# Kernel optimization log

Hardware: AMD Instinct MI355X
Metric: run time of the kernel (lower is better)

## Reference

```python
import jax, jax.numpy as jnp
import numpy as np

E = 8          # num_experts
K = 2          # top_k
D = 1024       # hidden_size
I = 4096       # intermediate_size
AUX_COEF = 0.02


def setup_inputs() -> dict:
    key = jax.random.key(0)
    ks = jax.random.split(key, 5)
    x = jax.random.normal(ks[0], (4, 2048, D), dtype=jnp.float32)
    w_gate = jax.random.normal(ks[1], (E, D), dtype=jnp.float32) * 0.02   # router, nn.Linear weight [E, D]
    wg = jax.random.normal(ks[2], (E, D, I), dtype=jnp.float32) * 0.02    # gate_proj per expert
    wu = jax.random.normal(ks[3], (E, D, I), dtype=jnp.float32) * 0.02    # up_proj per expert
    wd = jax.random.normal(ks[4], (E, I, D), dtype=jnp.float32) * 0.02    # down_proj per expert
    return {"x": x, "w_gate": w_gate, "wg": wg, "wu": wu, "wd": wd}


def reference(x, w_gate, wg, wu, wd):
    B, T, Dm = x.shape
    xf = x.reshape(-1, Dm)                                   # [N, D]
    N = xf.shape[0]

    # 1) Router: softmax (in fp32) + top-k, renormalize top-k weights
    logits = xf @ w_gate.T                                   # [N, E]
    probs = jax.nn.softmax(logits.astype(jnp.float32), axis=-1)
    topk_w, topk_idx = jax.lax.top_k(probs, K)               # [N, K]
    topk_w = (topk_w / topk_w.sum(-1, keepdims=True)).astype(x.dtype)

    # Per-expert combine weight (zero when expert not selected) — math-equivalent
    # to the original gather/scatter-add loop but jit-friendly and vectorized.
    onehot = jax.nn.one_hot(topk_idx, E, dtype=x.dtype)      # [N, K, E]
    combine = jnp.einsum('nk,nke->ne', topk_w, onehot)       # [N, E]

    # 2) Experts: SwiGLU FFN, combined with routing weights
    out = jnp.zeros_like(xf)
    for e in range(E):  # fixed small loop over structurally distinct experts
        h = jax.nn.silu(xf @ wg[e]) * (xf @ wu[e])           # [N, I]
        out = out + combine[:, e:e + 1] * (h @ wd[e])        # [N, D]

    # 3) Load-balancing aux loss (Switch Transformer)
    f = onehot.sum((0, 1)).astype(jnp.float32) / (N * K)     # dispatch fraction per expert
    p = probs.mean(0)                                        # mean routing prob per expert
    aux_loss = AUX_COEF * E * jnp.sum(f * p)

    return out.reshape(B, T, Dm), aux_loss
```

## Files before the change

### kernel.cpp

```cpp
#include <hip/hip_runtime.h>
#include <hip/hip_bf16.h>
#include <cstdint>
#include <cstddef>

#define NE 8
#define TK 2
#define DM 1024
#define IM 4096
#define NT 8192
#define NS (NT*TK)
#define SCAP (NS+256)

typedef __bf16 bf16_t;
typedef __bf16 bf16x8 __attribute__((ext_vector_type(8)));
typedef __bf16 bf16x4 __attribute__((ext_vector_type(4)));
typedef float f32x4 __attribute__((ext_vector_type(4)));

__device__ __forceinline__ void async_cp16(const bf16_t* g, bf16_t* l) {
  __builtin_amdgcn_global_load_lds(
      (__attribute__((address_space(1))) void*)(const_cast<bf16_t*>(g)),
      (__attribute__((address_space(3))) void*)(l), 16, 0, 0);
}

__global__ void transpose_cvt(const float* __restrict__ src, bf16_t* __restrict__ dst,
                              int R, int C) {
  __shared__ float t[32][33];
  int bx = blockIdx.x * 32, by = blockIdx.y * 32;
  size_t zb = (size_t)blockIdx.z * R * C;
  int tx = threadIdx.x, ty = threadIdx.y;
#pragma unroll
  for (int i = 0; i < 4; ++i)
    t[ty + i*8][tx] = src[zb + (size_t)(by + ty + i*8) * C + bx + tx];
  __syncthreads();
#pragma unroll
  for (int i = 0; i < 4; ++i)
    dst[zb + (size_t)(bx + ty + i*8) * R + by + tx] = (bf16_t)t[tx][ty + i*8];
}

__global__ void pack_gu(const float* __restrict__ wg, const float* __restrict__ wu,
                        bf16_t* __restrict__ Wgu) {
  __shared__ float t[32][33];
  int sel = blockIdx.z & 1, e = blockIdx.z >> 1;
  const float* src = sel ? wu : wg;
  size_t zb = (size_t)e * DM * IM;
  int bx = blockIdx.x * 32, by = blockIdx.y * 32;
  int tx = threadIdx.x, ty = threadIdx.y;
#pragma unroll
  for (int i = 0; i < 4; ++i)
    t[ty + i*8][tx] = src[zb + (size_t)(by + ty + i*8) * IM + bx + tx];
  __syncthreads();
#pragma unroll
  for (int i = 0; i < 4; ++i) {
    int icol = bx + ty + i*8;
    int p = ((icol >> 6) << 7) + (sel << 6) + (icol & 63);
    Wgu[((size_t)e * (2*IM) + p) * DM + by + tx] = (bf16_t)t[tx][ty + i*8];
  }
}

__global__ void router_kernel(const float* __restrict__ x, const float* __restrict__ wgate,
                              int* __restrict__ counts, float* __restrict__ prob_sum,
                              int* __restrict__ topk_idx, float* __restrict__ topk_w) {
  __shared__ float s_psum[NE];
  __shared__ int s_cnt[NE];
  int tid = threadIdx.x;
  if (tid < NE) { s_psum[tid] = 0.f; s_cnt[tid] = 0; }
  __syncthreads();
  int lane = tid & 63, wv = tid >> 6;
  for (int t = 0; t < 8; ++t) {
    int n = blockIdx.x * 32 + wv * 8 + t;
    float acc[NE];
#pragma unroll
    for (int e = 0; e < NE; ++e) acc[e] = 0.f;
#pragma unroll
    for (int j = 0; j < 16; ++j) {
      int d = j * 64 + lane;
      float xv = x[(size_t)n * DM + d];
#pragma unroll
      for (int e = 0; e < NE; ++e) acc[e] += xv * wgate[e * DM + d];
    }
#pragma unroll
    for (int e = 0; e < NE; ++e) {
#pragma unroll
      for (int off = 32; off > 0; off >>= 1) acc[e] += __shfl_xor(acc[e], off);
    }
    if (lane == 0) {
      float mx = acc[0];
#pragma unroll
      for (int e = 1; e < NE; ++e) mx = fmaxf(mx, acc[e]);
      float p[NE], s = 0.f;
#pragma unroll
      for (int e = 0; e < NE; ++e) { p[e] = __expf(acc[e] - mx); s += p[e]; }
      float inv = 1.f / s;
#pragma unroll
      for (int e = 0; e < NE; ++e) p[e] *= inv;
      int i0 = 0;
      for (int e = 1; e < NE; ++e) if (p[e] > p[i0]) i0 = e;
      int i1 = (i0 == 0) ? 1 : 0;
      for (int e = 0; e < NE; ++e) if (e != i0 && p[e] > p[i1]) i1 = e;
      float rs = 1.f / (p[i0] + p[i1]);
      topk_idx[n * 2 + 0] = i0; topk_idx[n * 2 + 1] = i1;
      topk_w[n * 2 + 0] = p[i0] * rs; topk_w[n * 2 + 1] = p[i1] * rs;
      atomicAdd(&s_cnt[i0], 1); atomicAdd(&s_cnt[i1], 1);
#pragma unroll
      for (int e = 0; e < NE; ++e) atomicAdd(&s_psum[e], p[e]);
    }
  }
  __syncthreads();
  if (tid < NE) { atomicAdd(&counts[tid], s_cnt[tid]); atomicAdd(&prob_sum[tid], s_psum[tid]); }
}

__global__ void scan_aux(const int* __restrict__ counts, const float* __restrict__ prob_sum,
                         int* __restrict__ offsets, int* __restrict__ cursors,
                         float* __restrict__ aux_out) {
  if (threadIdx.x == 0) {
    int off = 0;
    float aux = 0.f;
    for (int e = 0; e < NE; ++e) {
      offsets[e] = off; cursors[e] = off;
      float f = (float)counts[e] * (1.f / (float)NS);
      float p = prob_sum[e] * (1.f / (float)NT);
      aux += f * p;
      off += counts[e];
    }
    offsets[NE] = off;
    *aux_out = 0.02f * 8.f * aux;
  }
}

__global__ void gather_kernel(const float* __restrict__ x, const int* __restrict__ topk_idx,
                              const float* __restrict__ topk_w, int* __restrict__ cursors,
                              int* __restrict__ slot_token, float* __restrict__ slot_w,
                              int* __restrict__ pair_slot, bf16_t* __restrict__ Xg) {
  int lane = threadIdx.x & 63, wv = threadIdx.x >> 6;
  int pair = blockIdx.x * 4 + wv;
  int n = pair >> 1, k = pair & 1;
  int e = topk_idx[n * 2 + k];
  int slot = 0;
  if (lane == 0) slot = atomicAdd(&cursors[e], 1);
  slot = __shfl(slot, 0);
  if (lane == 0) {
    slot_token[slot] = n; slot_w[slot] = topk_w[n * 2 + k];
    pair_slot[pair] = slot;
  }
#pragma unroll
  for (int j = 0; j < 4; ++j) {
    int d4 = j * 256 + lane * 4;
    float4 v = *(const float4*)(x + (size_t)n * DM + d4);
    bf16x4 o;
    o[0] = (bf16_t)v.x; o[1] = (bf16_t)v.y; o[2] = (bf16_t)v.z; o[3] = (bf16_t)v.w;
    *(bf16x4*)(Xg + (size_t)slot * DM + d4) = o;
  }
}

#define MFMA16 __builtin_amdgcn_mfma_f32_16x16x32_bf16

__global__ __launch_bounds__(512, 2) void gemm1_kernel(
    const bf16_t* __restrict__ Xg, const bf16_t* __restrict__ Wgu,
    bf16_t* __restrict__ H, const int* __restrict__ offsets) {
  int e = blockIdx.z, mt = blockIdx.y, nt = blockIdx.x;
  int row0 = offsets[e], ne = offsets[e + 1] - row0;
  if (mt * 256 >= ne) return;
  int m0 = row0 + mt * 256;

  __shared__ bf16_t lds[2][4][128 * 64];

  int tid = threadIdx.x, lane = tid & 63, wv = tid >> 6;
  int fm = lane & 15, fq = lane >> 4;
  int wm = wv >> 2, wn = wv & 3;

  const bf16_t* Ab = Xg + (size_t)m0 * DM;
  const bf16_t* Bb = Wgu + ((size_t)e * (2 * IM) + nt * 256) * DM;

  int sr = tid >> 3;
  int sgc = ((tid & 7) ^ (sr & 7)) << 3;
  int sldo = tid * 8;

#define STAGE1(LDST, GBASE, COL) do {                                      \
    const bf16_t* _g = (GBASE);                                            \
    async_cp16(_g + (size_t)sr * DM + (COL) + sgc, (LDST) + sldo);         \
    async_cp16(_g + (size_t)(sr + 64) * DM + (COL) + sgc, (LDST) + sldo + 4096); \
  } while (0)

  int offA[4][2], offB[2][2];
#pragma unroll
  for (int m = 0; m < 4; ++m) {
    int r = m * 32 + wm * 16 + fm;
#pragma unroll
    for (int ks = 0; ks < 2; ++ks)
      offA[m][ks] = r * 64 + (((ks * 4 + fq) ^ (r & 7)) << 3);
  }
#pragma unroll
  for (int jh = 0; jh < 2; ++jh) {
    int r = jh * 64 + wn * 16 + fm;
#pragma unroll
    for (int ks = 0; ks < 2; ++ks)
      offB[jh][ks] = r * 64 + (((ks * 4 + fq) ^ (r & 7)) << 3);
  }

  f32x4 acc[8][4];
#pragma unroll
  for (int i = 0; i < 8; ++i)
#pragma unroll
    for (int j = 0; j < 4; ++j) acc[i][j] = (f32x4){0.f, 0.f, 0.f, 0.f};

  STAGE1(lds[0][0], Ab, 0);
  STAGE1(lds[0][2], Bb, 0);
  STAGE1(lds[0][3], Bb + (size_t)128 * DM, 0);
  STAGE1(lds[0][1], Ab + (size_t)128 * DM, 0);
  STAGE1(lds[1][0], Ab, 64);
  STAGE1(lds[1][2], Bb, 64);
  STAGE1(lds[1][3], Bb + (size_t)128 * DM, 64);
  asm volatile("s_waitcnt vmcnt(6)");
  __builtin_amdgcn_s_barrier();

  bf16x8 af[4][2], b0f[2][2], b1f[2][2];
#pragma unroll 1
  for (int t = 0; t < 16; ++t) {
    const int buf = t & 1;
    const bf16_t* LA0 = lds[buf][0];
    const bf16_t* LA1 = lds[buf][1];
    const bf16_t* LB0 = lds[buf][2];
    const bf16_t* LB1 = lds[buf][3];
#pragma unroll
    for (int m = 0; m < 4; ++m) {
      af[m][0] = *(const bf16x8*)(LA0 + offA[m][0]);
      af[m][1] = *(const bf16x8*)(LA0 + offA[m][1]);
    }
#pragma unroll
    for (int j = 0; j < 2; ++j) {
      b0f[j][0] = *(const bf16x8*)(LB0 + offB[j][0]);
      b0f[j][1] = *(const bf16x8*)(LB0 + offB[j][1]);
    }
    if (t + 1 < 16) STAGE1(lds[buf ^ 1][1], Ab + (size_t)128 * DM, (t + 1) * 64);
    __builtin_amdgcn_s_barrier();
    asm volatile("s_waitcnt lgkmcnt(0)");
    __builtin_amdgcn_sched_barrier(0);
    __builtin_amdgcn_s_setprio(1);
#pragma unroll
    for (int m = 0; m < 4; ++m)
#pragma unroll
      for (int j = 0; j < 2; ++j) {
        acc[m][j] = MFMA16(af[m][0], b0f[j][0], acc[m][j], 0, 0, 0);
        acc[m][j] = MFMA16(af[m][1], b0f[j][1], acc[m][j], 0, 0, 0);
      }
    __builtin_amdgcn_s_setprio(0);
    __builtin_amdgcn_s_barrier();
#pragma unroll
    for (int j = 0; j < 2; ++j) {
      b1f[j][0] = *(const bf16x8*)(LB1 + offB[j][0]);
      b1f[j][1] = *(const bf16x8*)(LB1 + offB[j][1]);
    }
    if (t + 2 < 16) STAGE1(lds[buf][0], Ab, (t + 2) * 64);
    __builtin_amdgcn_s_barrier();
    asm volatile("s_waitcnt lgkmcnt(0)");
    __builtin_amdgcn_sched_barrier(0);
    __builtin_amdgcn_s_setprio(1);
#pragma unroll
    for (int m = 0; m < 4; ++m)
#pragma unroll
      for (int j = 0; j < 2; ++j) {
        acc[m][2 + j] = MFMA16(af[m][0], b1f[j][0], acc[m][2 + j], 0, 0, 0);
        acc[m][2 + j] = MFMA16(af[m][1], b1f[j][1], acc[m][2 + j], 0, 0, 0);
      }
    __builtin_amdgcn_s_setprio(0);
    __builtin_amdgcn_s_barrier();
#pragma unroll
    for (int m = 0; m < 4; ++m) {
      af[m][0] = *(const bf16x8*)(LA1 + offA[m][0]);
      af[m][1] = *(const bf16x8*)(LA1 + offA[m][1]);
    }
    if (t + 2 < 16) STAGE1(lds[buf][2], Bb, (t + 2) * 64);
    __builtin_amdgcn_s_barrier();
    asm volatile("s_waitcnt lgkmcnt(0)");
    __builtin_amdgcn_sched_barrier(0);
    __builtin_amdgcn_s_setprio(1);
#pragma unroll
    for (int m = 0; m < 4; ++m)
#pragma unroll
      for (int j = 0; j < 2; ++j) {
        acc[4 + m][j] = MFMA16(af[m][0], b0f[j][0], acc[4 + m][j], 0, 0, 0);
        acc[4 + m][j] = MFMA16(af[m][1], b0f[j][1], acc[4 + m][j], 0, 0, 0);
      }
    __builtin_amdgcn_s_setprio(0);
    __builtin_amdgcn_s_barrier();
    if (t + 2 < 16) STAGE1(lds[buf][3], Bb + (size_t)128 * DM, (t + 2) * 64);
    if (t < 14) { asm volatile("s_waitcnt vmcnt(6)"); }
    else if (t == 14) { asm volatile("s_waitcnt vmcnt(0)"); }
    __builtin_amdgcn_s_barrier();
    __builtin_amdgcn_s_setprio(1);
#pragma unroll
    for (int m = 0; m < 4; ++m)
#pragma unroll
      for (int j = 0; j < 2; ++j) {
        acc[4 + m][2 + j] = MFMA16(af[m][0], b1f[j][0], acc[4 + m][2 + j], 0, 0, 0);
        acc[4 + m][2 + j] = MFMA16(af[m][1], b1f[j][1], acc[4 + m][2 + j], 0, 0, 0);
      }
    __builtin_amdgcn_s_setprio(0);
    __builtin_amdgcn_s_barrier();
  }
#undef STAGE1

#pragma unroll
  for (int i = 0; i < 8; ++i) {
    int lr = i * 32 + wm * 16 + fq * 4;
#pragma unroll
    for (int rr = 0; rr < 4; ++rr) {
      if (mt * 256 + lr + rr < ne) {
        bf16_t* hp = H + (size_t)(m0 + lr + rr) * IM + nt * 128 + wn * 16 + fm;
        float g0 = acc[i][0][rr], u0 = acc[i][1][rr];
        hp[0] = (bf16_t)(g0 * __builtin_amdgcn_rcpf(1.f + __expf(-g0)) * u0);
        float g1 = acc[i][2][rr], u1 = acc[i][3][rr];
        hp[64] = (bf16_t)(g1 * __builtin_amdgcn_rcpf(1.f + __expf(-g1)) * u1);
      }
    }
  }
}

__global__ __launch_bounds__(256, 2) void gemm2_kernel(
    const bf16_t* __restrict__ H, const bf16_t* __restrict__ Wdt,
    const int* __restrict__ offsets, bf16_t* __restrict__ Y) {
  int e = blockIdx.z, mt = blockIdx.y, nt = blockIdx.x;
  int row0 = offsets[e], ne = offsets[e + 1] - row0;
  if (mt * 128 >= ne) return;
  int m0 = row0 + mt * 128;
  int n0 = nt * 128;

  __shared__ bf16_t sA[128 * 64];
  __shared__ bf16_t sB[128 * 64];

  int tid = threadIdx.x, lane = tid & 63, wv = tid >> 6;
  int fm = lane & 15, fq = lane >> 4;
  int wm = (wv & 1) * 64, wn = (wv >> 1) * 64;

  f32x4 acc[4][4];
#pragma unroll
  for (int i = 0; i < 4; ++i)
#pragma unroll
    for (int j = 0; j < 4; ++j) acc[i][j] = (f32x4){0.f, 0.f, 0.f, 0.f};

  const bf16_t* Ab = H + (size_t)m0 * IM;
  const bf16_t* Bb = Wdt + ((size_t)e * DM + n0) * IM;

  for (int k0 = 0; k0 < IM; k0 += 64) {
    __syncthreads();
#pragma unroll
    for (int it = 0; it < 4; ++it) {
      int c = it * 256 + tid;
      int r = c >> 3, c8 = c & 7;
      int gc8 = c8 ^ (r & 7);
      size_t go = (size_t)r * IM + k0 + gc8 * 8;
      async_cp16(Ab + go, sA + c * 8);
      async_cp16(Bb + go, sB + c * 8);
    }
    __syncthreads();
#pragma unroll
    for (int s = 0; s < 2; ++s) {
      bf16x8 af[4], bf[4];
      int q = s * 4 + fq;
#pragma unroll
      for (int i = 0; i < 4; ++i) {
        int ra = wm + i * 16 + fm;
        int rb = wn + i * 16 + fm;
        af[i] = *(const bf16x8*)(sA + ra * 64 + (q ^ (ra & 7)) * 8);
        bf[i] = *(const bf16x8*)(sB + rb * 64 + (q ^ (rb & 7)) * 8);
      }
#pragma unroll
      for (int i = 0; i < 4; ++i)
#pragma unroll
        for (int j = 0; j < 4; ++j)
          acc[i][j] = __builtin_amdgcn_mfma_f32_16x16x32_bf16(af[i], bf[j], acc[i][j], 0, 0, 0);
    }
  }
#pragma unroll
  for (int i = 0; i < 4; ++i) {
#pragma unroll
    for (int r = 0; r < 4; ++r) {
      int lm = wm + i * 16 + fq * 4 + r;
      if (mt * 128 + lm < ne) {
        bf16_t* yrow = Y + (size_t)(m0 + lm) * DM + n0 + wn;
#pragma unroll
        for (int j = 0; j < 4; ++j)
          yrow[j * 16 + fm] = (bf16_t)acc[i][j][r];
      }
    }
  }
}

__global__ void combine_kernel(const bf16_t* __restrict__ Y, const int* __restrict__ pair_slot,
                               const float* __restrict__ topk_w, float* __restrict__ out) {
  int n = blockIdx.x;
  int t = threadIdx.x;
  int s0 = pair_slot[n * 2 + 0], s1 = pair_slot[n * 2 + 1];
  float w0 = topk_w[n * 2 + 0], w1 = topk_w[n * 2 + 1];
  bf16x4 y0 = *(const bf16x4*)(Y + (size_t)s0 * DM + t * 4);
  bf16x4 y1 = *(const bf16x4*)(Y + (size_t)s1 * DM + t * 4);
  float4 o;
  o.x = w0 * (float)y0[0] + w1 * (float)y1[0];
  o.y = w0 * (float)y0[1] + w1 * (float)y1[1];
  o.z = w0 * (float)y0[2] + w1 * (float)y1[2];
  o.w = w0 * (float)y0[3] + w1 * (float)y1[3];
  *(float4*)(out + (size_t)n * DM + t * 4) = o;
}

static constexpr size_t OFF_TOPKI = 256;
static constexpr size_t OFF_TOPKW = OFF_TOPKI + (size_t)NT * 2 * 4;
static constexpr size_t OFF_STOK  = OFF_TOPKW + (size_t)NT * 2 * 4;
static constexpr size_t OFF_SW    = OFF_STOK + (size_t)NS * 4;
static constexpr size_t OFF_PSLOT = OFF_SW + (size_t)NS * 4;
static constexpr size_t OFF_XG    = OFF_PSLOT + (size_t)NS * 4;
static constexpr size_t OFF_H     = OFF_XG + (size_t)SCAP * DM * 2;
static constexpr size_t OFF_WGU   = OFF_H + (size_t)SCAP * IM * 2;
static constexpr size_t OFF_WDT   = OFF_WGU + (size_t)NE * 2 * IM * DM * 2;

extern "C" void kernel_launch(void* const* d_in, const int* in_sizes, int n_in,
                              void* d_out, int out_size, void* d_ws, size_t ws_size,
                              hipStream_t stream) {
  const float* x      = (const float*)d_in[0];
  const float* w_gate = (const float*)d_in[1];
  const float* wg     = (const float*)d_in[2];
  const float* wu     = (const float*)d_in[3];
  const float* wd     = (const float*)d_in[4];
  float* out = (float*)d_out;

  char* ws = (char*)d_ws;
  int*   counts   = (int*)(ws + 0);
  int*   cursors  = (int*)(ws + 32);
  int*   offsets  = (int*)(ws + 64);
  float* prob_sum = (float*)(ws + 128);
  int*   topk_idx = (int*)(ws + OFF_TOPKI);
  float* topk_w   = (float*)(ws + OFF_TOPKW);
  int*   slot_tok = (int*)(ws + OFF_STOK);
  float* slot_w   = (float*)(ws + OFF_SW);
  int*   pair_slot= (int*)(ws + OFF_PSLOT);
  bf16_t* Xg  = (bf16_t*)(ws + OFF_XG);
  bf16_t* Yb  = Xg;
  bf16_t* Hb  = (bf16_t*)(ws + OFF_H);
  bf16_t* Wgu = (bf16_t*)(ws + OFF_WGU);
  bf16_t* Wdt = (bf16_t*)(ws + OFF_WDT);

  hipMemsetAsync(ws, 0, 256, stream);

  pack_gu<<<dim3(IM / 32, DM / 32, NE * 2), dim3(32, 8), 0, stream>>>(wg, wu, Wgu);
  transpose_cvt<<<dim3(DM / 32, IM / 32, NE), dim3(32, 8), 0, stream>>>(wd, Wdt, IM, DM);

  router_kernel<<<NT / 32, 256, 0, stream>>>(x, w_gate, counts, prob_sum, topk_idx, topk_w);
  scan_aux<<<1, 64, 0, stream>>>(counts, prob_sum, offsets, cursors, out + (out_size - 1));
  gather_kernel<<<NS / 4, 256, 0, stream>>>(x, topk_idx, topk_w, cursors, slot_tok, slot_w,
                                            pair_slot, Xg);

  gemm1_kernel<<<dim3(IM / 128, 64, NE), 512, 0, stream>>>(Xg, Wgu, Hb, offsets);
  gemm2_kernel<<<dim3(DM / 128, 64, NE), 256, 0, stream>>>(Hb, Wdt, offsets, Yb);
  combine_kernel<<<NT, 256, 0, stream>>>(Yb, pair_slot, topk_w, out);
}
```

Measured before the change: 1.234 ms.

## Unify MoE GEMMs into templated pipelined kernel with compact tile list

After: 1.183 ms. -4.1%, faster.

```diff
diff --git a/kernel.cpp b/kernel.cpp
--- a/kernel.cpp
+++ b/kernel.cpp
@@ -10,6 +10,7 @@
 #define NT 8192
 #define NS (NT*TK)
 #define SCAP (NS+256)
+#define MAXT 72
 
 typedef __bf16 bf16_t;
 typedef __bf16 bf16x8 __attribute__((ext_vector_type(8)));
@@ -111,18 +112,28 @@
 
 __global__ void scan_aux(const int* __restrict__ counts, const float* __restrict__ prob_sum,
                          int* __restrict__ offsets, int* __restrict__ cursors,
-                         float* __restrict__ aux_out) {
+                         float* __restrict__ aux_out, int* __restrict__ tl_m0,
+                         int* __restrict__ tl_e, int* __restrict__ tl_rows,
+                         int* __restrict__ n_tiles) {
   if (threadIdx.x == 0) {
     int off = 0;
     float aux = 0.f;
+    int t = 0;
     for (int e = 0; e < NE; ++e) {
       offsets[e] = off; cursors[e] = off;
-      float f = (float)counts[e] * (1.f / (float)NS);
+      int c = counts[e];
+      float f = (float)c * (1.f / (float)NS);
       float p = prob_sum[e] * (1.f / (float)NT);
       aux += f * p;
-      off += counts[e];
+      for (int m = 0; m * 256 < c && t < MAXT; ++m, ++t) {
+        tl_m0[t] = off + m * 256;
+        tl_e[t] = e;
+        tl_rows[t] = min(256, c - m * 256);
+      }
+      off += c;
     }
     offsets[NE] = off;
+    *n_tiles = t;
     *aux_out = 0.02f * 8.f * aux;
   }
 }
@@ -153,14 +164,22 @@
 }
 
 #define MFMA16 __builtin_amdgcn_mfma_f32_16x16x32_bf16
-
-__global__ __launch_bounds__(512, 2) void gemm1_kernel(
-    const bf16_t* __restrict__ Xg, const bf16_t* __restrict__ Wgu,
-    bf16_t* __restrict__ H, const int* __restrict__ offsets) {
-  int e = blockIdx.z, mt = blockIdx.y, nt = blockIdx.x;
-  int row0 = offsets[e], ne = offsets[e + 1] - row0;
-  if (mt * 256 >= ne) return;
-  int m0 = row0 + mt * 256;
+#define SBAR  __builtin_amdgcn_s_barrier
+#define SCHED __builtin_amdgcn_sched_barrier
+#define PRIO  __builtin_amdgcn_s_setprio
+
+template<int NTK, int KSTR, int BROWS, bool SWIGLU>
+__global__ __launch_bounds__(512, 2) void moe_gemm(
+    const bf16_t* __restrict__ A, const bf16_t* __restrict__ Bw,
+    bf16_t* __restrict__ O,
+    const int* __restrict__ tl_m0, const int* __restrict__ tl_e,
+    const int* __restrict__ tl_rows, const int* __restrict__ n_tiles) {
+  int ty = blockIdx.y;
+  if (ty >= *n_tiles) return;
+  int m0 = tl_m0[ty];
+  int e  = tl_e[ty];
+  int rows = tl_rows[ty];
+  int nt = blockIdx.x;
 
   __shared__ bf16_t lds[2][4][128 * 64];
 
@@ -168,17 +187,17 @@
   int fm = lane & 15, fq = lane >> 4;
   int wm = wv >> 2, wn = wv & 3;
 
-  const bf16_t* Ab = Xg + (size_t)m0 * DM;
-  const bf16_t* Bb = Wgu + ((size_t)e * (2 * IM) + nt * 256) * DM;
+  const bf16_t* Ab = A + (size_t)m0 * KSTR;
+  const bf16_t* Bb = Bw + ((size_t)e * BROWS + (size_t)nt * 256) * KSTR;
 
   int sr = tid >> 3;
   int sgc = ((tid & 7) ^ (sr & 7)) << 3;
   int sldo = tid * 8;
 
-#define STAGE1(LDST, GBASE, COL) do {                                      \
+#define STG(LDST, GBASE, COL) do {                                         \
     const bf16_t* _g = (GBASE);                                            \
-    async_cp16(_g + (size_t)sr * DM + (COL) + sgc, (LDST) + sldo);         \
-    async_cp16(_g + (size_t)(sr + 64) * DM + (COL) + sgc, (LDST) + sldo + 4096); \
+    async_cp16(_g + (size_t)sr * KSTR + (COL) + sgc, (LDST) + sldo);       \
+    async_cp16(_g + (size_t)(sr + 64) * KSTR + (COL) + sgc, (LDST) + sldo + 4096); \
   } while (0)
 
   int offA[4][2], offB[2][2];
@@ -203,39 +222,48 @@
 #pragma unroll
     for (int j = 0; j < 4; ++j) acc[i][j] = (f32x4){0.f, 0.f, 0.f, 0.f};
 
-  STAGE1(lds[0][0], Ab, 0);
-  STAGE1(lds[0][2], Bb, 0);
-  STAGE1(lds[0][3], Bb + (size_t)128 * DM, 0);
-  STAGE1(lds[0][1], Ab + (size_t)128 * DM, 0);
-  STAGE1(lds[1][0], Ab, 64);
-  STAGE1(lds[1][2], Bb, 64);
-  STAGE1(lds[1][3], Bb + (size_t)128 * DM, 64);
+  STG(lds[0][0], Ab, 0);
+  STG(lds[0][2], Bb, 0);
+  STG(lds[0][3], Bb + (size_t)128 * KSTR, 0);
+  STG(lds[0][1], Ab + (size_t)128 * KSTR, 0);
+  STG(lds[1][0], Ab, 64);
+  STG(lds[1][2], Bb, 64);
+  STG(lds[1][3], Bb + (size_t)128 * KSTR, 64);
   asm volatile("s_waitcnt vmcnt(6)");
-  __builtin_amdgcn_s_barrier();
+  SBAR();
+  SCHED(0);
 
   bf16x8 af[4][2], b0f[2][2], b1f[2][2];
+#pragma unroll
+  for (int j = 0; j < 2; ++j) {
+    b0f[j][0] = *(const bf16x8*)(lds[0][2] + offB[j][0]);
+    b0f[j][1] = *(const bf16x8*)(lds[0][2] + offB[j][1]);
+  }
+#pragma unroll
+  for (int m = 0; m < 4; ++m) {
+    af[m][0] = *(const bf16x8*)(lds[0][0] + offA[m][0]);
+    af[m][1] = *(const bf16x8*)(lds[0][0] + offA[m][1]);
+  }
+  SCHED(0);
+
 #pragma unroll 1
-  for (int t = 0; t < 16; ++t) {
+  for (int t = 0; t < NTK; ++t) {
     const int buf = t & 1;
-    const bf16_t* LA0 = lds[buf][0];
     const bf16_t* LA1 = lds[buf][1];
-    const bf16_t* LB0 = lds[buf][2];
     const bf16_t* LB1 = lds[buf][3];
-#pragma unroll
-    for (int m = 0; m < 4; ++m) {
-      af[m][0] = *(const bf16x8*)(LA0 + offA[m][0]);
-      af[m][1] = *(const bf16x8*)(LA0 + offA[m][1]);
-    }
+    const bf16_t* NA0 = lds[buf ^ 1][0];
+    const bf16_t* NB0 = lds[buf ^ 1][2];
+    if (t + 1 < NTK) STG(lds[buf ^ 1][1], Ab + (size_t)128 * KSTR, (t + 1) * 64);
 #pragma unroll
     for (int j = 0; j < 2; ++j) {
-      b0f[j][0] = *(const bf16x8*)(LB0 + offB[j][0]);
-      b0f[j][1] = *(const bf16x8*)(LB0 + offB[j][1]);
-    }
-    if (t + 1 < 16) STAGE1(lds[buf ^ 1][1], Ab + (size_t)128 * DM, (t + 1) * 64);
-    __builtin_amdgcn_s_barrier();
-    asm volatile("s_waitcnt lgkmcnt(0)");
-    __builtin_amdgcn_sched_barrier(0);
-    __builtin_amdgcn_s_setprio(1);
+      b1f[j][0] = *(const bf16x8*)(LB1 + offB[j][0]);
+      b1f[j][1] = *(const bf16x8*)(LB1 + offB[j][1]);
+    }
+    SCHED(0);
+    asm volatile("s_waitcnt lgkmcnt(4)");
+    SBAR();
+    SCHED(0);
+    PRIO(1);
 #pragma unroll
     for (int m = 0; m < 4; ++m)
 #pragma unroll
@@ -243,18 +271,14 @@
         acc[m][j] = MFMA16(af[m][0], b0f[j][0], acc[m][j], 0, 0, 0);
         acc[m][j] = MFMA16(af[m][1], b0f[j][1], acc[m][j], 0, 0, 0);
       }
-    __builtin_amdgcn_s_setprio(0);
-    __builtin_amdgcn_s_barrier();
-#pragma unroll
-    for (int j = 0; j < 2; ++j) {
-      b1f[j][0] = *(const bf16x8*)(LB1 + offB[j][0]);
-      b1f[j][1] = *(const bf16x8*)(LB1 + offB[j][1]);
-    }
-    if (t + 2 < 16) STAGE1(lds[buf][0], Ab, (t + 2) * 64);
-    __builtin_amdgcn_s_barrier();
+    PRIO(0);
+    SCHED(0);
+    if (t + 2 < NTK) STG(lds[buf][0], Ab, (t + 2) * 64);
+    SCHED(0);
     asm volatile("s_waitcnt lgkmcnt(0)");
-    __builtin_amdgcn_sched_barrier(0);
-    __builtin_amdgcn_s_setprio(1);
+    SBAR();
+    SCHED(0);
+    PRIO(1);
 #pragma unroll
     for (int m = 0; m < 4; ++m)
 #pragma unroll
@@ -262,18 +286,20 @@
         acc[m][2 + j] = MFMA16(af[m][0], b1f[j][0], acc[m][2 + j], 0, 0, 0);
         acc[m][2 + j] = MFMA16(af[m][1], b1f[j][1], acc[m][2 + j], 0, 0, 0);
       }
-    __builtin_amdgcn_s_setprio(0);
-    __builtin_amdgcn_s_barrier();
+    PRIO(0);
+    SCHED(0);
 #pragma unroll
     for (int m = 0; m < 4; ++m) {
       af[m][0] = *(const bf16x8*)(LA1 + offA[m][0]);
       af[m][1] = *(const bf16x8*)(LA1 + offA[m][1]);
     }
-    if (t + 2 < 16) STAGE1(lds[buf][2], Bb, (t + 2) * 64);
-    __builtin_amdgcn_s_barrier();
+    SCHED(0);
+    if (t + 2 < NTK) STG(lds[buf][2], Bb, (t + 2) * 64);
+    SCHED(0);
     asm volatile("s_waitcnt lgkmcnt(0)");
-    __builtin_amdgcn_sched_barrier(0);
-    __builtin_amdgcn_s_setprio(1);
+    SBAR();
+    SCHED(0);
+    PRIO(1);
 #pragma unroll
     for (int m = 0; m < 4; ++m)
 #pragma unroll
@@ -281,13 +307,23 @@
         acc[4 + m][j] = MFMA16(af[m][0], b0f[j][0], acc[4 + m][j], 0, 0, 0);
         acc[4 + m][j] = MFMA16(af[m][1], b0f[j][1], acc[4 + m][j], 0, 0, 0);
       }
-    __builtin_amdgcn_s_setprio(0);
-    __builtin_amdgcn_s_barrier();
-    if (t + 2 < 16) STAGE1(lds[buf][3], Bb + (size_t)128 * DM, (t + 2) * 64);
-    if (t < 14) { asm volatile("s_waitcnt vmcnt(6)"); }
-    else if (t == 14) { asm volatile("s_waitcnt vmcnt(0)"); }
-    __builtin_amdgcn_s_barrier();
-    __builtin_amdgcn_s_setprio(1);
+    PRIO(0);
+    SCHED(0);
+    if (t + 2 < NTK) STG(lds[buf][3], Bb + (size_t)128 * KSTR, (t + 2) * 64);
+    SCHED(0);
+    if (t < NTK - 2)       { asm volatile("s_waitcnt vmcnt(6)"); }
+    else if (t == NTK - 2) { asm volatile("s_waitcnt vmcnt(0)"); }
+    SBAR();
+    SCHED(0);
+    if (t + 1 < NTK) {
+#pragma unroll
+      for (int j = 0; j < 2; ++j) {
+        b0f[j][0] = *(const bf16x8*)(NB0 + offB[j][0]);
+        b0f[j][1] = *(const bf16x8*)(NB0 + offB[j][1]);
+      }
+    }
+    SCHED(0);
+    PRIO(1);
 #pragma unroll
     for (int m = 0; m < 4; ++m)
 #pragma unroll
@@ -295,92 +331,38 @@
         acc[4 + m][2 + j] = MFMA16(af[m][0], b1f[j][0], acc[4 + m][2 + j], 0, 0, 0);
         acc[4 + m][2 + j] = MFMA16(af[m][1], b1f[j][1], acc[4 + m][2 + j], 0, 0, 0);
       }
-    __builtin_amdgcn_s_setprio(0);
-    __builtin_amdgcn_s_barrier();
-  }
-#undef STAGE1
+    PRIO(0);
+    SCHED(0);
+    if (t + 1 < NTK) {
+#pragma unroll
+      for (int m = 0; m < 4; ++m) {
+        af[m][0] = *(const bf16x8*)(NA0 + offA[m][0]);
+        af[m][1] = *(const bf16x8*)(NA0 + offA[m][1]);
+      }
+    }
+    SCHED(0);
+  }
+#undef STG
 
 #pragma unroll
   for (int i = 0; i < 8; ++i) {
     int lr = i * 32 + wm * 16 + fq * 4;
 #pragma unroll
     for (int rr = 0; rr < 4; ++rr) {
-      if (mt * 256 + lr + rr < ne) {
-        bf16_t* hp = H + (size_t)(m0 + lr + rr) * IM + nt * 128 + wn * 16 + fm;
-        float g0 = acc[i][0][rr], u0 = acc[i][1][rr];
-        hp[0] = (bf16_t)(g0 * __builtin_amdgcn_rcpf(1.f + __expf(-g0)) * u0);
-        float g1 = acc[i][2][rr], u1 = acc[i][3][rr];
-        hp[64] = (bf16_t)(g1 * __builtin_amdgcn_rcpf(1.f + __expf(-g1)) * u1);
-      }
-    }
-  }
-}
-
-__global__ __launch_bounds__(256, 2) void gemm2_kernel(
-    const bf16_t* __restrict__ H, const bf16_t* __restrict__ Wdt,
-    const int* __restrict__ offsets, bf16_t* __restrict__ Y) {
-  int e = blockIdx.z, mt = blockIdx.y, nt = blockIdx.x;
-  int row0 = offsets[e], ne = offsets[e + 1] - row0;
-  if (mt * 128 >= ne) return;
-  int m0 = row0 + mt * 128;
-  int n0 = nt * 128;
-
-  __shared__ bf16_t sA[128 * 64];
-  __shared__ bf16_t sB[128 * 64];
-
-  int tid = threadIdx.x, lane = tid & 63, wv = tid >> 6;
-  int fm = lane & 15, fq = lane >> 4;
-  int wm = (wv & 1) * 64, wn = (wv >> 1) * 64;
-
-  f32x4 acc[4][4];
-#pragma unroll
-  for (int i = 0; i < 4; ++i)
-#pragma unroll
-    for (int j = 0; j < 4; ++j) acc[i][j] = (f32x4){0.f, 0.f, 0.f, 0.f};
-
-  const bf16_t* Ab = H + (size_t)m0 * IM;
-  const bf16_t* Bb = Wdt + ((size_t)e * DM + n0) * IM;
-
-  for (int k0 = 0; k0 < IM; k0 += 64) {
-    __syncthreads();
-#pragma unroll
-    for (int it = 0; it < 4; ++it) {
-      int c = it * 256 + tid;
-      int r = c >> 3, c8 = c & 7;
-      int gc8 = c8 ^ (r & 7);
-      size_t go = (size_t)r * IM + k0 + gc8 * 8;
-      async_cp16(Ab + go, sA + c * 8);
-      async_cp16(Bb + go, sB + c * 8);
-    }
-    __syncthreads();
-#pragma unroll
-    for (int s = 0; s < 2; ++s) {
-      bf16x8 af[4], bf[4];
-      int q = s * 4 + fq;
-#pragma unroll
-      for (int i = 0; i < 4; ++i) {
-        int ra = wm + i * 16 + fm;
-        int rb = wn + i * 16 + fm;
-        af[i] = *(const bf16x8*)(sA + ra * 64 + (q ^ (ra & 7)) * 8);
-        bf[i] = *(const bf16x8*)(sB + rb * 64 + (q ^ (rb & 7)) * 8);
-      }
-#pragma unroll
-      for (int i = 0; i < 4; ++i)
-#pragma unroll
-        for (int j = 0; j < 4; ++j)
-          acc[i][j] = __builtin_amdgcn_mfma_f32_16x16x32_bf16(af[i], bf[j], acc[i][j], 0, 0, 0);
-    }
-  }
-#pragma unroll
-  for (int i = 0; i < 4; ++i) {
-#pragma unroll
-    for (int r = 0; r < 4; ++r) {
-      int lm = wm + i * 16 + fq * 4 + r;
-      if (mt * 128 + lm < ne) {
-        bf16_t* yrow = Y + (size_t)(m0 + lm) * DM + n0 + wn;
-#pragma unroll
-        for (int j = 0; j < 4; ++j)
-          yrow[j * 16 + fm] = (bf16_t)acc[i][j][r];
+      if (lr + rr < rows) {
+        if constexpr (SWIGLU) {
+          bf16_t* hp = O + (size_t)(m0 + lr + rr) * IM + nt * 128 + wn * 16 + fm;
+          float g0 = acc[i][0][rr], u0 = acc[i][1][rr];
+          hp[0] = (bf16_t)(g0 * __builtin_amdgcn_rcpf(1.f + __expf(-g0)) * u0);
+          float g1 = acc[i][2][rr], u1 = acc[i][3][rr];
+          hp[64] = (bf16_t)(g1 * __builtin_amdgcn_rcpf(1.f + __expf(-g1)) * u1);
+        } else {
+          bf16_t* yp = O + (size_t)(m0 + lr + rr) * DM + nt * 256 + wn * 16 + fm;
+          yp[0]   = (bf16_t)acc[i][0][rr];
+          yp[64]  = (bf16_t)acc[i][1][rr];
+          yp[128] = (bf16_t)acc[i][2][rr];
+          yp[192] = (bf16_t)acc[i][3][rr];
+        }
       }
     }
   }
@@ -402,7 +384,11 @@
   *(float4*)(out + (size_t)n * DM + t * 4) = o;
 }
 
-static constexpr size_t OFF_TOPKI = 256;
+static constexpr size_t OFF_TL    = 256;
+static constexpr size_t OFF_TLE   = OFF_TL  + (size_t)MAXT * 4;
+static constexpr size_t OFF_TLR   = OFF_TLE + (size_t)MAXT * 4;
+static constexpr size_t OFF_NTL   = OFF_TLR + (size_t)MAXT * 4;
+static constexpr size_t OFF_TOPKI = 1536;
 static constexpr size_t OFF_TOPKW = OFF_TOPKI + (size_t)NT * 2 * 4;
 static constexpr size_t OFF_STOK  = OFF_TOPKW + (size_t)NT * 2 * 4;
 static constexpr size_t OFF_SW    = OFF_STOK + (size_t)NS * 4;
@@ -427,6 +413,10 @@
   int*   cursors  = (int*)(ws + 32);
   int*   offsets  = (int*)(ws + 64);
   float* prob_sum = (float*)(ws + 128);
+  int*   tl_m0    = (int*)(ws + OFF_TL);
+  int*   tl_e     = (int*)(ws + OFF_TLE);
+  int*   tl_rows  = (int*)(ws + OFF_TLR);
+  int*   n_tiles  = (int*)(ws + OFF_NTL);
   int*   topk_idx = (int*)(ws + OFF_TOPKI);
   float* topk_w   = (float*)(ws + OFF_TOPKW);
   int*   slot_tok = (int*)(ws + OFF_STOK);
@@ -444,11 +434,15 @@
   transpose_cvt<<<dim3(DM / 32, IM / 32, NE), dim3(32, 8), 0, stream>>>(wd, Wdt, IM, DM);
 
   router_kernel<<<NT / 32, 256, 0, stream>>>(x, w_gate, counts, prob_sum, topk_idx, topk_w);
-  scan_aux<<<1, 64, 0, stream>>>(counts, prob_sum, offsets, cursors, out + (out_size - 1));
+  scan_aux<<<1, 64, 0, stream>>>(counts, prob_sum, offsets, cursors, out + (out_size - 1),
+                                 tl_m0, tl_e, tl_rows, n_tiles);
   gather_kernel<<<NS / 4, 256, 0, stream>>>(x, topk_idx, topk_w, cursors, slot_tok, slot_w,
                                             pair_slot, Xg);
 
-  gemm1_kernel<<<dim3(IM / 128, 64, NE), 512, 0, stream>>>(Xg, Wgu, Hb, offsets);
-  gemm2_kernel<<<dim3(DM / 128, 64, NE), 256, 0, stream>>>(Hb, Wdt, offsets, Yb);
+  moe_gemm<DM / 64, DM, 2 * IM, true><<<dim3(32, MAXT), 512, 0, stream>>>(
+      Xg, Wgu, Hb, tl_m0, tl_e, tl_rows, n_tiles);
+  moe_gemm<IM / 64, IM, DM, false><<<dim3(4, MAXT), 512, 0, stream>>>(
+      Hb, Wdt, Yb, tl_m0, tl_e, tl_rows, n_tiles);
+
   combine_kernel<<<NT, 256, 0, stream>>>(Yb, pair_slot, topk_w, out);
 }
```
